# Kernel tuning notes

Hardware: AMD Instinct MI355X
Metric: run time of the kernel (lower is better)

Reference implementation:

```python
import jax, jax.numpy as jnp
import numpy as np

V = 50000   # vocab_size == output_size
E = 256     # emb_size
H = 512     # hidden_size
B = 128     # batch_size
L = 400     # encoder seq len
T = 100     # decoder history len


def setup_inputs() -> dict:
    key = jax.random.key(0)
    ks = jax.random.split(key, 20)
    s = 0.02
    return {
        "inputs": jax.random.randint(ks[0], (1, B), 0, V),
        "hidden": jax.random.normal(ks[1], (1, B, H), jnp.float32),
        "encoder_hidden": jax.random.normal(ks[2], (L, B, H), jnp.float32),
        "encoder_lengths": jax.random.randint(ks[3], (B,), 0, L),
        "previous_weights": jax.random.normal(ks[4], (B, 1, L), jnp.float32),
        "decoder_hidden": jax.random.normal(ks[5], (T, B, H), jnp.float32),
        "encoder_inputs": jax.random.randint(ks[6], (L, B), 0, V),
        "time_step": 0,
        "emb": jax.random.normal(ks[7], (V, E), jnp.float32) * s,
        "W_ih": jax.random.normal(ks[8], (3 * H, E), jnp.float32) * s,
        "W_hh": jax.random.normal(ks[9], (3 * H, H), jnp.float32) * s,
        "b_ih": jnp.zeros((3 * H,), jnp.float32),
        "b_hh": jnp.zeros((3 * H,), jnp.float32),
        "W_ae": jax.random.normal(ks[10], (H, H), jnp.float32) * s,
        "b_ae": jnp.zeros((H,), jnp.float32),
        "W_ad": jax.random.normal(ks[11], (H, H), jnp.float32) * s,
        "b_ad": jnp.zeros((H,), jnp.float32),
        "W_ptr": jax.random.normal(ks[12], (1, 3 * H), jnp.float32) * s,
        "b_ptr": jnp.zeros((1,), jnp.float32),
        "W_out": jax.random.normal(ks[13], (V, 3 * H), jnp.float32) * s,
        "b_out": jnp.zeros((V,), jnp.float32),
    }


def _gru_step(x, h, W_ih, W_hh, b_ih, b_hh):
    # Single-step torch-style GRU. x: (B,E), h: (B,H)
    hsz = h.shape[-1]
    gi = x @ W_ih.T + b_ih          # (B, 3H)
    gh = h @ W_hh.T + b_hh          # (B, 3H)
    i_r, i_z, i_n = gi[:, :hsz], gi[:, hsz:2 * hsz], gi[:, 2 * hsz:]
    h_r, h_z, h_n = gh[:, :hsz], gh[:, hsz:2 * hsz], gh[:, 2 * hsz:]
    r = jax.nn.sigmoid(i_r + h_r)
    z = jax.nn.sigmoid(i_z + h_z)
    n = jnp.tanh(i_n + r * h_n)
    return (1.0 - z) * n + z * h


def reference(inputs, hidden, encoder_hidden, encoder_lengths, previous_weights,
              decoder_hidden, encoder_inputs, time_step,
              emb, W_ih, W_hh, b_ih, b_hh, W_ae, b_ae, W_ad, b_ad,
              W_ptr, b_ptr, W_out, b_out):
    x = emb[inputs[0]]                       # (B,E)
    h = _gru_step(x, hidden[0], W_ih, W_hh, b_ih, b_hh)   # (B,H) == h_t_d

    enc_len = encoder_hidden.shape[0]
    # encoder attention
    te = h @ W_ae.T + b_ae                   # (B,H)
    e_t = jnp.einsum('bh,lbh->bl', te, encoder_hidden)    # (B,L)
    # faithful reproduction of source mask loop (empty slice -> effectively no-op)
    cond = (enc_len < encoder_lengths)[:, None] & (jnp.arange(enc_len)[None, :] >= encoder_lengths[:, None])
    e_t = jnp.where(cond, -jnp.inf, e_t)
    alpha_e = jax.nn.softmax(e_t, axis=-1)                # (B,L)
    c_t_e = jnp.einsum('bl,lbh->bh', alpha_e, encoder_hidden)

    # decoder (intra) attention
    td = h @ W_ad.T + b_ad
    e_t_d = jnp.einsum('bh,tbh->bt', td, decoder_hidden)  # (B,T)
    alpha_d = jax.nn.softmax(e_t_d, axis=-1)
    c_t_d = jnp.einsum('bt,tbh->bh', alpha_d, decoder_hidden)

    new_hidden = jnp.concatenate([c_t_e, h, c_t_d], axis=-1)   # (B,3H)
    gen = jax.nn.log_softmax(new_hidden @ W_out.T + b_out, axis=-1)  # (B,V)
    pointer_prob = new_hidden @ W_ptr.T + b_ptr                      # (B,1)

    enc_in = encoder_inputs.T                                        # (B,L) int
    alpha_scaled = pointer_prob * alpha_e                            # (B,L)
    vsz = W_out.shape[0]
    bidx = jnp.arange(enc_in.shape[0])[:, None]
    pointer_mask = jnp.zeros((enc_in.shape[0], vsz), gen.dtype).at[bidx, enc_in].add(alpha_scaled)

    final_output = (1.0 - pointer_prob) * gen + pointer_mask         # (B,V)
    return final_output, h[None], previous_weights
```

## Files before the change

### kernel.cpp

```cpp
#include <hip/hip_runtime.h>
#include <cstdint>
#include <cstddef>

#define VV 50000
#define EE 256
#define HH 512
#define BB 128
#define LL 400
#define TT 100
#define H3 1536

typedef __attribute__((ext_vector_type(8))) short short8;
typedef __attribute__((ext_vector_type(4))) float floatx4;

__device__ __forceinline__ unsigned short f2bf(float x) {
    union { float f; unsigned u; } v; v.f = x;
    unsigned r = v.u + 0x7fffu + ((v.u >> 16) & 1u);
    return (unsigned short)(r >> 16);
}

struct GemmJob {
    const float* A;
    const float* W;
    const float* bias;
    float*       C;
    int          lda;
    int          K;
};

#define GBN 64
#define GBK 32

__global__ __launch_bounds__(256) void gemm_m128(GemmJob j0, GemmJob j1,
                                                 int N, int ldc)
{
    GemmJob j = (blockIdx.y == 0) ? j0 : j1;
    __shared__ float As[GBK][128];
    __shared__ float Wls[GBK][GBN];

    const int tid = threadIdx.x;
    const int n0  = blockIdx.x * GBN;
    const int tx  = tid & 15;
    const int ty  = tid >> 4;
    const int kq  = tid & 7;
    const int arow = (tid >> 3) * 4;
    const int wrow = (tid >> 3) * 2;

    float acc[8][4];
    #pragma unroll
    for (int i = 0; i < 8; i++)
        #pragma unroll
        for (int jj = 0; jj < 4; jj++) acc[i][jj] = 0.f;

    for (int k0 = 0; k0 < j.K; k0 += GBK) {
        #pragma unroll
        for (int i = 0; i < 4; i++) {
            const float4 v = *(const float4*)(j.A + (size_t)(arow + i) * j.lda + k0 + kq * 4);
            As[kq*4+0][arow+i] = v.x;
            As[kq*4+1][arow+i] = v.y;
            As[kq*4+2][arow+i] = v.z;
            As[kq*4+3][arow+i] = v.w;
        }
        #pragma unroll
        for (int i = 0; i < 2; i++) {
            const int n = n0 + wrow + i;
            float4 v = make_float4(0.f, 0.f, 0.f, 0.f);
            if (n < N) v = *(const float4*)(j.W + (size_t)n * j.K + k0 + kq * 4);
            Wls[kq*4+0][wrow+i] = v.x;
            Wls[kq*4+1][wrow+i] = v.y;
            Wls[kq*4+2][wrow+i] = v.z;
            Wls[kq*4+3][wrow+i] = v.w;
        }
        __syncthreads();
        #pragma unroll
        for (int kk = 0; kk < GBK; kk++) {
            float a[8], w[4];
            #pragma unroll
            for (int i = 0; i < 8; i++) a[i] = As[kk][ty*8+i];
            #pragma unroll
            for (int jj = 0; jj < 4; jj++) w[jj] = Wls[kk][tx*4+jj];
            #pragma unroll
            for (int i = 0; i < 8; i++)
                #pragma unroll
                for (int jj = 0; jj < 4; jj++)
                    acc[i][jj] += a[i] * w[jj];
        }
        __syncthreads();
    }

    const int nbase = n0 + tx * 4;
    #pragma unroll
    for (int i = 0; i < 8; i++) {
        const int b = ty * 8 + i;
        if (nbase + 3 < N) {
            const float4 bb = *(const float4*)(j.bias + nbase);
            float4 r;
            r.x = acc[i][0] + bb.x;
            r.y = acc[i][1] + bb.y;
            r.z = acc[i][2] + bb.z;
            r.w = acc[i][3] + bb.w;
            *(float4*)(j.C + (size_t)b * ldc + nbase) = r;
        } else {
            #pragma unroll
            for (int jj = 0; jj < 4; jj++) {
                const int n = nbase + jj;
                if (n < N) j.C[(size_t)b * ldc + n] = acc[i][jj] + j.bias[n];
            }
        }
    }
}

__global__ __launch_bounds__(256) void vocab_mfma(const unsigned short* __restrict__ A,
                                                  const float* __restrict__ W,
                                                  const float* __restrict__ bias,
                                                  float* __restrict__ C)
{
    const int wave = threadIdx.x >> 6;
    const int lane = threadIdx.x & 63;
    const int quad = lane >> 4;
    const int nl   = lane & 15;
    const int n    = blockIdx.x * 64 + wave * 16 + nl;
    const int nc   = (n < VV) ? n : (VV - 1);

    floatx4 acc[8];
    #pragma unroll
    for (int i = 0; i < 8; i++) acc[i] = (floatx4){0.f, 0.f, 0.f, 0.f};

    const float* wp = W + (size_t)nc * H3 + quad * 8;
    const unsigned short* ap = A + (size_t)nl * H3 + quad * 8;

    for (int k0 = 0; k0 < H3; k0 += 32) {
        const float4 w0 = *(const float4*)(wp + k0);
        const float4 w1 = *(const float4*)(wp + k0 + 4);
        short8 bfrag;
        bfrag[0] = (short)f2bf(w0.x);
        bfrag[1] = (short)f2bf(w0.y);
        bfrag[2] = (short)f2bf(w0.z);
        bfrag[3] = (short)f2bf(w0.w);
        bfrag[4] = (short)f2bf(w1.x);
        bfrag[5] = (short)f2bf(w1.y);
        bfrag[6] = (short)f2bf(w1.z);
        bfrag[7] = (short)f2bf(w1.w);
        #pragma unroll
        for (int mt = 0; mt < 8; mt++) {
            const short8 af = *(const short8*)(ap + (size_t)mt * 16 * H3 + k0);
            acc[mt] = __builtin_amdgcn_mfma_f32_16x16x32_bf16(af, bfrag, acc[mt], 0, 0, 0);
        }
    }

    if (n < VV) {
        const float bv = bias[n];
        #pragma unroll
        for (int mt = 0; mt < 8; mt++) {
            #pragma unroll
            for (int r = 0; r < 4; r++) {
                const int m = mt * 16 + quad * 4 + r;
                C[(size_t)m * VV + n] = acc[mt][r] + bv;
            }
        }
    }
}

__global__ __launch_bounds__(256) void nh_to_bf16(const float* __restrict__ nh,
                                                  unsigned short* __restrict__ out)
{
    const int idx = blockIdx.x * 256 + threadIdx.x;
    out[idx] = f2bf(nh[idx]);
}

__global__ __launch_bounds__(256) void gather_emb(const int* __restrict__ tok,
                                                  const float* __restrict__ emb,
                                                  float* __restrict__ x)
{
    const int b = blockIdx.x;
    x[(size_t)b * EE + threadIdx.x] = emb[(size_t)tok[b] * EE + threadIdx.x];
}

__global__ __launch_bounds__(256) void zero_ctx(float* __restrict__ nh)
{
    float* p = nh + (size_t)blockIdx.x * H3;
    const int tid = threadIdx.x;
    p[tid] = 0.f;  p[tid + 256] = 0.f;
    p[1024 + tid] = 0.f;  p[1280 + tid] = 0.f;
}

__global__ __launch_bounds__(256) void gru_combine(const float* __restrict__ gi,
                                                   const float* __restrict__ gh,
                                                   const float* __restrict__ hprev,
                                                   float* __restrict__ nh,
                                                   float* __restrict__ out_h)
{
    const int b = blockIdx.x;
    const int tid = threadIdx.x;
    #pragma unroll
    for (int r = 0; r < 2; r++) {
        const int i = tid + r * 256;
        const size_t base = (size_t)b * H3;
        const float ir = gi[base + i],        hr = gh[base + i];
        const float iz = gi[base + 512 + i],  hz = gh[base + 512 + i];
        const float in_ = gi[base + 1024 + i], hn = gh[base + 1024 + i];
        const float rr = 1.f / (1.f + expf(-(ir + hr)));
        const float zz = 1.f / (1.f + expf(-(iz + hz)));
        const float nn = tanhf(in_ + rr * hn);
        const float hp = hprev[(size_t)b * HH + i];
        const float h  = (1.f - zz) * nn + zz * hp;
        nh[base + 512 + i] = h;
        out_h[(size_t)b * HH + i] = h;
    }
}

__global__ __launch_bounds__(256) void attn_scores(const float* __restrict__ q,
                                                   const float* __restrict__ ctx,
                                                   const int* __restrict__ lens,
                                                   float* __restrict__ out,
                                                   int Lc)
{
    const int b = blockIdx.y;
    const int wave = threadIdx.x >> 6;
    const int lane = threadIdx.x & 63;
    const int l = blockIdx.x * 4 + wave;
    const float4* q4 = (const float4*)(q + (size_t)b * HH);
    const float4* c4 = (const float4*)(ctx + ((size_t)l * BB + b) * HH);
    const float4 a0 = q4[lane],      b0 = c4[lane];
    const float4 a1 = q4[lane + 64], b1 = c4[lane + 64];
    float s = a0.x*b0.x + a0.y*b0.y + a0.z*b0.z + a0.w*b0.w
            + a1.x*b1.x + a1.y*b1.y + a1.z*b1.z + a1.w*b1.w;
    #pragma unroll
    for (int off = 32; off; off >>= 1)
        s += __shfl_down(s, off);
    if (lane == 0) {
        if (lens && (Lc < lens[b]) && (l >= lens[b])) s = -__builtin_inff();
        out[(size_t)b * Lc + l] = s;
    }
}

__global__ __launch_bounds__(256) void softmax2(float* __restrict__ ae, int ne,
                                                float* __restrict__ ad, int nd)
{
    __shared__ float red[256];
    const int tid = threadIdx.x;
    float* row;
    int n;
    if (blockIdx.y == 0) { row = ae + (size_t)blockIdx.x * ne; n = ne; }
    else                 { row = ad + (size_t)blockIdx.x * nd; n = nd; }

    float m = -__builtin_inff();
    for (int i = tid; i < n; i += 256) m = fmaxf(m, row[i]);
    red[tid] = m; __syncthreads();
    for (int s = 128; s; s >>= 1) {
        if (tid < s) red[tid] = fmaxf(red[tid], red[tid + s]);
        __syncthreads();
    }
    m = red[0]; __syncthreads();

    float sum = 0.f;
    for (int i = tid; i < n; i += 256) sum += expf(row[i] - m);
    red[tid] = sum; __syncthreads();
    for (int s = 128; s; s >>= 1) {
        if (tid < s) red[tid] += red[tid + s];
        __syncthreads();
    }
    const float inv = 1.f / red[0];
    for (int i = tid; i < n; i += 256) row[i] = expf(row[i] - m) * inv;
}

__global__ __launch_bounds__(256) void attn_context(const float* __restrict__ alpha,
                                                    const float* __restrict__ ctx,
                                                    float* __restrict__ dst,
                                                    int Lc, int chunk, int off)
{
    __shared__ float al[32];
    const int b = blockIdx.y;
    const int l0 = blockIdx.x * chunk;
    const int tid = threadIdx.x;
    if (tid < chunk) al[tid] = alpha[(size_t)b * Lc + l0 + tid];
    __syncthreads();
    float ax = 0.f, ay = 0.f;
    for (int ll = 0; ll < chunk; ll++) {
        const float2* c = (const float2*)(ctx + ((size_t)(l0 + ll) * BB + b) * HH);
        const float2 v = c[tid];
        const float w = al[ll];
        ax += w * v.x;
        ay += w * v.y;
    }
    atomicAdd(&dst[(size_t)b * H3 + off + tid * 2 + 0], ax);
    atomicAdd(&dst[(size_t)b * H3 + off + tid * 2 + 1], ay);
}

__global__ __launch_bounds__(256) void pointer_kernel(const float* __restrict__ nh,
                                                      const float* __restrict__ W_ptr,
                                                      const float* __restrict__ b_ptr,
                                                      float* __restrict__ pp)
{
    __shared__ float red[256];
    const int b = blockIdx.x;
    const int tid = threadIdx.x;
    float s = 0.f;
    for (int jj = tid; jj < H3; jj += 256) s += nh[(size_t)b * H3 + jj] * W_ptr[jj];
    red[tid] = s; __syncthreads();
    for (int t = 128; t; t >>= 1) {
        if (tid < t) red[tid] += red[tid + t];
        __syncthreads();
    }
    if (tid == 0) pp[b] = red[0] + b_ptr[0];
}

#define LSE_CHUNKS 10
#define LSE_SPAN 5000

__global__ __launch_bounds__(256) void lse_part(const float* __restrict__ logits,
                                                float2* __restrict__ part)
{
    __shared__ float rm[256], rs[256];
    const int b = blockIdx.y;
    const int s = blockIdx.x;
    const int tid = threadIdx.x;
    const float4* row = (const float4*)(logits + (size_t)b * VV + (size_t)s * LSE_SPAN);
    float m = -__builtin_inff(), sum = 0.f;
    for (int i = tid; i < LSE_SPAN / 4; i += 256) {
        const float4 v = row[i];
        const float mx = fmaxf(fmaxf(v.x, v.y), fmaxf(v.z, v.w));
        if (mx > m) { sum *= expf(m - mx); m = mx; }
        sum += expf(v.x - m) + expf(v.y - m) + expf(v.z - m) + expf(v.w - m);
    }
    rm[tid] = m; rs[tid] = sum; __syncthreads();
    for (int t = 128; t; t >>= 1) {
        if (tid < t) {
            const float m2 = rm[tid + t], s2 = rs[tid + t];
            const float M = fmaxf(rm[tid], m2);
            rs[tid] = rs[tid] * expf(rm[tid] - M) + s2 * expf(m2 - M);
            rm[tid] = M;
        }
        __syncthreads();
    }
    if (tid == 0) part[(size_t)b * LSE_CHUNKS + s] = make_float2(rm[0], rs[0]);
}

__global__ __launch_bounds__(128) void lse_final(const float2* __restrict__ part,
                                                 float* __restrict__ lse)
{
    const int b = threadIdx.x;
    float m = -__builtin_inff(), s = 0.f;
    #pragma unroll
    for (int i = 0; i < LSE_CHUNKS; i++) {
        const float2 p = part[(size_t)b * LSE_CHUNKS + i];
        const float M = fmaxf(m, p.x);
        s = s * expf(m - M) + p.y * expf(p.x - M);
        m = M;
    }
    lse[b] = m + logf(s);
}

__global__ __launch_bounds__(256) void final_write(float* __restrict__ out,
                                                   const float* __restrict__ pp,
                                                   const float* __restrict__ lse)
{
    const int b = blockIdx.y;
    const int v = (blockIdx.x * 256 + threadIdx.x) * 4;
    if (v >= VV) return;
    float4* p = (float4*)(out + (size_t)b * VV + v);
    float4 x = *p;
    const float g = 1.f - pp[b];
    const float Lse = lse[b];
    x.x = g * (x.x - Lse);
    x.y = g * (x.y - Lse);
    x.z = g * (x.z - Lse);
    x.w = g * (x.w - Lse);
    *p = x;
}

__global__ __launch_bounds__(256) void scatter_pointer(float* __restrict__ out,
                                                       const float* __restrict__ pp,
                                                       const float* __restrict__ alpha_e,
                                                       const int* __restrict__ enc_in)
{
    const int idx = blockIdx.x * 256 + threadIdx.x;
    if (idx >= BB * LL) return;
    const int b = idx / LL;
    const int l = idx - b * LL;
    const int tok = enc_in[(size_t)l * BB + b];
    atomicAdd(&out[(size_t)b * VV + tok], pp[b] * alpha_e[idx]);
}

__global__ __launch_bounds__(256) void copy_pw(float* __restrict__ dst,
                                               const float* __restrict__ src)
{
    const int idx = blockIdx.x * 256 + threadIdx.x;
    if (idx < BB * LL) dst[idx] = src[idx];
}

extern "C" void kernel_launch(void* const* d_in, const int* in_sizes, int n_in,
                              void* d_out, int out_size, void* d_ws, size_t ws_size,
                              hipStream_t stream)
{
    const int*   inputs  = (const int*)  d_in[0];
    const float* hidden  = (const float*)d_in[1];
    const float* enc_h   = (const float*)d_in[2];
    const int*   enc_len = (const int*)  d_in[3];
    const float* prev_w  = (const float*)d_in[4];
    const float* dec_h   = (const float*)d_in[5];
    const int*   enc_in  = (const int*)  d_in[6];
    const float* emb     = (const float*)d_in[8];
    const float* W_ih    = (const float*)d_in[9];
    const float* W_hh    = (const float*)d_in[10];
    const float* b_ih    = (const float*)d_in[11];
    const float* b_hh    = (const float*)d_in[12];
    const float* W_ae    = (const float*)d_in[13];
    const float* b_ae    = (const float*)d_in[14];
    const float* W_ad    = (const float*)d_in[15];
    const float* b_ad    = (const float*)d_in[16];
    const float* W_ptr   = (const float*)d_in[17];
    const float* b_ptr   = (const float*)d_in[18];
    const float* W_out   = (const float*)d_in[19];
    const float* b_out   = (const float*)d_in[20];

    float* out = (float*)d_out;
    float* out_final = out;
    float* out_h     = out + (size_t)BB * VV;
    float* out_pw    = out_h + (size_t)BB * HH;

    float* ws  = (float*)d_ws;
    float* X   = ws;
    float* GI  = X   + BB * EE;
    float* GH  = GI  + BB * H3;
    float* TE  = GH  + BB * H3;
    float* TD  = TE  + BB * HH;
    float* AE  = TD  + BB * HH;
    float* AD  = AE  + BB * LL;
    float* NH  = AD  + BB * TT;
    float* PP  = NH  + BB * H3;
    float* LSE = PP  + BB;
    float2* PART = (float2*)(LSE + BB);
    unsigned short* ABF = (unsigned short*)(PART + BB * LSE_CHUNKS);

    gather_emb<<<BB, 256, 0, stream>>>(inputs, emb, X);
    zero_ctx<<<BB, 256, 0, stream>>>(NH);

    {
        GemmJob jgi{X,      W_ih, b_ih, GI, EE, EE};
        GemmJob jgh{hidden, W_hh, b_hh, GH, HH, HH};
        gemm_m128<<<dim3(H3 / GBN, 2), 256, 0, stream>>>(jgi, jgh, H3, H3);
    }
    gru_combine<<<BB, 256, 0, stream>>>(GI, GH, hidden, NH, out_h);

    {
        GemmJob jte{NH + 512, W_ae, b_ae, TE, H3, HH};
        GemmJob jtd{NH + 512, W_ad, b_ad, TD, H3, HH};
        gemm_m128<<<dim3(HH / GBN, 2), 256, 0, stream>>>(jte, jtd, HH, HH);
    }

    attn_scores<<<dim3(LL / 4, BB), 256, 0, stream>>>(TE, enc_h, enc_len, AE, LL);
    attn_scores<<<dim3(TT / 4, BB), 256, 0, stream>>>(TD, dec_h, nullptr, AD, TT);

    softmax2<<<dim3(BB, 2), 256, 0, stream>>>(AE, LL, AD, TT);

    attn_context<<<dim3(LL / 25, BB), 256, 0, stream>>>(AE, enc_h, NH, LL, 25, 0);
    attn_context<<<dim3(TT / 25, BB), 256, 0, stream>>>(AD, dec_h, NH, TT, 25, 1024);

    pointer_kernel<<<BB, 256, 0, stream>>>(NH, W_ptr, b_ptr, PP);

    nh_to_bf16<<<(BB * H3) / 256, 256, 0, stream>>>(NH, ABF);
    vocab_mfma<<<(VV + 63) / 64, 256, 0, stream>>>(ABF, W_out, b_out, out_final);

    lse_part<<<dim3(LSE_CHUNKS, BB), 256, 0, stream>>>(out_final, PART);
    lse_final<<<1, 128, 0, stream>>>(PART, LSE);
    final_write<<<dim3((VV / 4 + 255) / 256, BB), 256, 0, stream>>>(out_final, PP, LSE);

    scatter_pointer<<<(BB * LL) / 256, 256, 0, stream>>>(out_final, PP, AE, enc_in);

    copy_pw<<<(BB * LL) / 256, 256, 0, stream>>>(out_pw, prev_w);
}
```

Measured before the change: 907.6 us.

## Fuse small kernels and software-pipeline loads in vocab MFMA GEMM

Merges several small launches: gather and zeroing into one prep kernel, encoder and decoder attention score and context kernels into single launches, the bf16 conversion into the pointer kernel, lse_final into final_write, and the prev-weights copy into the scatter. The vocab projection GEMM now prefetches the next K-slice of weights and activations into registers before issuing the current MFMAs, and packs fp32 to bf16 with a byte-permute. The bf16 packing changes from round-to-nearest-even to round-half-up, which slightly alters rounding. Every row block in final_write now recomputes the log-sum-exp combine redundantly.

```diff
diff --git a/kernel.cpp b/kernel.cpp
--- a/kernel.cpp
+++ b/kernel.cpp
@@ -17,6 +17,14 @@
     union { float f; unsigned u; } v; v.f = x;
     unsigned r = v.u + 0x7fffu + ((v.u >> 16) & 1u);
     return (unsigned short)(r >> 16);
+}
+
+__device__ __forceinline__ unsigned bfpack(float x, float y) {
+    union { float f; unsigned u; } a, b;
+    a.f = x; b.f = y;
+    const unsigned lo = a.u + 0x8000u;
+    const unsigned hi = b.u + 0x8000u;
+    return __builtin_amdgcn_perm(hi, lo, 0x07060302u);
 }
 
 struct GemmJob {
@@ -129,23 +137,37 @@
     const float* wp = W + (size_t)nc * H3 + quad * 8;
     const unsigned short* ap = A + (size_t)nl * H3 + quad * 8;
 
+    float4 cw0 = *(const float4*)(wp);
+    float4 cw1 = *(const float4*)(wp + 4);
+    short8 caf[8];
+    #pragma unroll
+    for (int mt = 0; mt < 8; mt++)
+        caf[mt] = *(const short8*)(ap + (size_t)mt * 16 * H3);
+
     for (int k0 = 0; k0 < H3; k0 += 32) {
-        const float4 w0 = *(const float4*)(wp + k0);
-        const float4 w1 = *(const float4*)(wp + k0 + 4);
-        short8 bfrag;
-        bfrag[0] = (short)f2bf(w0.x);
-        bfrag[1] = (short)f2bf(w0.y);
-        bfrag[2] = (short)f2bf(w0.z);
-        bfrag[3] = (short)f2bf(w0.w);
-        bfrag[4] = (short)f2bf(w1.x);
-        bfrag[5] = (short)f2bf(w1.y);
-        bfrag[6] = (short)f2bf(w1.z);
-        bfrag[7] = (short)f2bf(w1.w);
-        #pragma unroll
-        for (int mt = 0; mt < 8; mt++) {
-            const short8 af = *(const short8*)(ap + (size_t)mt * 16 * H3 + k0);
-            acc[mt] = __builtin_amdgcn_mfma_f32_16x16x32_bf16(af, bfrag, acc[mt], 0, 0, 0);
-        }
+        int k1 = k0 + 32;
+        k1 = (k1 < H3) ? k1 : 0;
+        const float4 nw0 = *(const float4*)(wp + k1);
+        const float4 nw1 = *(const float4*)(wp + k1 + 4);
+        short8 naf[8];
+        #pragma unroll
+        for (int mt = 0; mt < 8; mt++)
+            naf[mt] = *(const short8*)(ap + (size_t)mt * 16 * H3 + k1);
+
+        int4 bi;
+        bi.x = (int)bfpack(cw0.x, cw0.y);
+        bi.y = (int)bfpack(cw0.z, cw0.w);
+        bi.z = (int)bfpack(cw1.x, cw1.y);
+        bi.w = (int)bfpack(cw1.z, cw1.w);
+        const short8 bf = *(const short8*)&bi;
+
+        #pragma unroll
+        for (int mt = 0; mt < 8; mt++)
+            acc[mt] = __builtin_amdgcn_mfma_f32_16x16x32_bf16(caf[mt], bf, acc[mt], 0, 0, 0);
+
+        cw0 = nw0; cw1 = nw1;
+        #pragma unroll
+        for (int mt = 0; mt < 8; mt++) caf[mt] = naf[mt];
     }
 
     if (n < VV) {
@@ -161,25 +183,15 @@
     }
 }
 
-__global__ __launch_bounds__(256) void nh_to_bf16(const float* __restrict__ nh,
-                                                  unsigned short* __restrict__ out)
-{
-    const int idx = blockIdx.x * 256 + threadIdx.x;
-    out[idx] = f2bf(nh[idx]);
-}
-
-__global__ __launch_bounds__(256) void gather_emb(const int* __restrict__ tok,
-                                                  const float* __restrict__ emb,
-                                                  float* __restrict__ x)
+__global__ __launch_bounds__(256) void prep(const int* __restrict__ tok,
+                                            const float* __restrict__ emb,
+                                            float* __restrict__ x,
+                                            float* __restrict__ nh)
 {
     const int b = blockIdx.x;
-    x[(size_t)b * EE + threadIdx.x] = emb[(size_t)tok[b] * EE + threadIdx.x];
-}
-
-__global__ __launch_bounds__(256) void zero_ctx(float* __restrict__ nh)
-{
-    float* p = nh + (size_t)blockIdx.x * H3;
-    const int tid = threadIdx.x;
+    const int tid = threadIdx.x;
+    x[(size_t)b * EE + tid] = emb[(size_t)tok[b] * EE + tid];
+    float* p = nh + (size_t)b * H3;
     p[tid] = 0.f;  p[tid + 256] = 0.f;
     p[1024 + tid] = 0.f;  p[1280 + tid] = 0.f;
 }
@@ -209,18 +221,33 @@
     }
 }
 
-__global__ __launch_bounds__(256) void attn_scores(const float* __restrict__ q,
-                                                   const float* __restrict__ ctx,
-                                                   const int* __restrict__ lens,
-                                                   float* __restrict__ out,
-                                                   int Lc)
+__global__ __launch_bounds__(256) void attn_scores2(const float* __restrict__ qe,
+                                                    const float* __restrict__ ctxe,
+                                                    const int* __restrict__ lens,
+                                                    float* __restrict__ oute,
+                                                    const float* __restrict__ qd,
+                                                    const float* __restrict__ ctxd,
+                                                    float* __restrict__ outd)
 {
     const int b = blockIdx.y;
     const int wave = threadIdx.x >> 6;
     const int lane = threadIdx.x & 63;
-    const int l = blockIdx.x * 4 + wave;
+
+    const float* q;
+    const float* c;
+    float* o;
+    int l, Lc;
+    bool mask;
+    if (blockIdx.x < 100) {
+        l = blockIdx.x * 4 + wave; Lc = LL;
+        q = qe; c = ctxe; o = oute; mask = true;
+    } else {
+        l = (blockIdx.x - 100) * 4 + wave; Lc = TT;
+        q = qd; c = ctxd; o = outd; mask = false;
+    }
+
     const float4* q4 = (const float4*)(q + (size_t)b * HH);
-    const float4* c4 = (const float4*)(ctx + ((size_t)l * BB + b) * HH);
+    const float4* c4 = (const float4*)(c + ((size_t)l * BB + b) * HH);
     const float4 a0 = q4[lane],      b0 = c4[lane];
     const float4 a1 = q4[lane + 64], b1 = c4[lane + 64];
     float s = a0.x*b0.x + a0.y*b0.y + a0.z*b0.z + a0.w*b0.w
@@ -229,8 +256,8 @@
     for (int off = 32; off; off >>= 1)
         s += __shfl_down(s, off);
     if (lane == 0) {
-        if (lens && (Lc < lens[b]) && (l >= lens[b])) s = -__builtin_inff();
-        out[(size_t)b * Lc + l] = s;
+        if (mask && (Lc < lens[b]) && (l >= lens[b])) s = -__builtin_inff();
+        o[(size_t)b * Lc + l] = s;
     }
 }
 
@@ -264,19 +291,32 @@
     for (int i = tid; i < n; i += 256) row[i] = expf(row[i] - m) * inv;
 }
 
-__global__ __launch_bounds__(256) void attn_context(const float* __restrict__ alpha,
-                                                    const float* __restrict__ ctx,
-                                                    float* __restrict__ dst,
-                                                    int Lc, int chunk, int off)
+__global__ __launch_bounds__(256) void attn_context2(const float* __restrict__ ae,
+                                                     const float* __restrict__ ctxe,
+                                                     const float* __restrict__ ad,
+                                                     const float* __restrict__ ctxd,
+                                                     float* __restrict__ dst)
 {
     __shared__ float al[32];
     const int b = blockIdx.y;
-    const int l0 = blockIdx.x * chunk;
-    const int tid = threadIdx.x;
-    if (tid < chunk) al[tid] = alpha[(size_t)b * Lc + l0 + tid];
+    const int tid = threadIdx.x;
+
+    const float* alpha;
+    const float* ctx;
+    int l0, Lc, off;
+    if (blockIdx.x < 16) {
+        l0 = blockIdx.x * 25; Lc = LL; off = 0;
+        alpha = ae; ctx = ctxe;
+    } else {
+        l0 = (blockIdx.x - 16) * 25; Lc = TT; off = 1024;
+        alpha = ad; ctx = ctxd;
+    }
+
+    if (tid < 25) al[tid] = alpha[(size_t)b * Lc + l0 + tid];
     __syncthreads();
     float ax = 0.f, ay = 0.f;
-    for (int ll = 0; ll < chunk; ll++) {
+    #pragma unroll 5
+    for (int ll = 0; ll < 25; ll++) {
         const float2* c = (const float2*)(ctx + ((size_t)(l0 + ll) * BB + b) * HH);
         const float2 v = c[tid];
         const float w = al[ll];
@@ -287,16 +327,23 @@
     atomicAdd(&dst[(size_t)b * H3 + off + tid * 2 + 1], ay);
 }
 
-__global__ __launch_bounds__(256) void pointer_kernel(const float* __restrict__ nh,
-                                                      const float* __restrict__ W_ptr,
-                                                      const float* __restrict__ b_ptr,
-                                                      float* __restrict__ pp)
+__global__ __launch_bounds__(256) void pointer_bf16(const float* __restrict__ nh,
+                                                    const float* __restrict__ W_ptr,
+                                                    const float* __restrict__ b_ptr,
+                                                    float* __restrict__ pp,
+                                                    unsigned short* __restrict__ abf)
 {
     __shared__ float red[256];
     const int b = blockIdx.x;
     const int tid = threadIdx.x;
     float s = 0.f;
-    for (int jj = tid; jj < H3; jj += 256) s += nh[(size_t)b * H3 + jj] * W_ptr[jj];
+    #pragma unroll
+    for (int r = 0; r < 6; r++) {
+        const int jj = tid + r * 256;
+        const float v = nh[(size_t)b * H3 + jj];
+        abf[(size_t)b * H3 + jj] = f2bf(v);
+        s += v * W_ptr[jj];
+    }
     red[tid] = s; __syncthreads();
     for (int t = 128; t; t >>= 1) {
         if (tid < t) red[tid] += red[tid + t];
@@ -336,10 +383,11 @@
     if (tid == 0) part[(size_t)b * LSE_CHUNKS + s] = make_float2(rm[0], rs[0]);
 }
 
-__global__ __launch_bounds__(128) void lse_final(const float2* __restrict__ part,
-                                                 float* __restrict__ lse)
-{
-    const int b = threadIdx.x;
+__global__ __launch_bounds__(256) void final_write(float* __restrict__ out,
+                                                   const float* __restrict__ pp,
+                                                   const float2* __restrict__ part)
+{
+    const int b = blockIdx.y;
     float m = -__builtin_inff(), s = 0.f;
     #pragma unroll
     for (int i = 0; i < LSE_CHUNKS; i++) {
@@ -348,20 +396,13 @@
         s = s * expf(m - M) + p.y * expf(p.x - M);
         m = M;
     }
-    lse[b] = m + logf(s);
-}
-
-__global__ __launch_bounds__(256) void final_write(float* __restrict__ out,
-                                                   const float* __restrict__ pp,
-                                                   const float* __restrict__ lse)
-{
-    const int b = blockIdx.y;
+    const float Lse = m + logf(s);
+
     const int v = (blockIdx.x * 256 + threadIdx.x) * 4;
     if (v >= VV) return;
     float4* p = (float4*)(out + (size_t)b * VV + v);
     float4 x = *p;
     const float g = 1.f - pp[b];
-    const float Lse = lse[b];
     x.x = g * (x.x - Lse);
     x.y = g * (x.y - Lse);
     x.z = g * (x.z - Lse);
@@ -369,24 +410,20 @@
     *p = x;
 }
 
-__global__ __launch_bounds__(256) void scatter_pointer(float* __restrict__ out,
-                                                       const float* __restrict__ pp,
-                                                       const float* __restrict__ alpha_e,
-                                                       const int* __restrict__ enc_in)
+__global__ __launch_bounds__(256) void scatter_copy(float* __restrict__ out,
+                                                    const float* __restrict__ pp,
+                                                    const float* __restrict__ alpha_e,
+                                                    const int* __restrict__ enc_in,
+                                                    float* __restrict__ pw_dst,
+                                                    const float* __restrict__ pw_src)
 {
     const int idx = blockIdx.x * 256 + threadIdx.x;
     if (idx >= BB * LL) return;
+    pw_dst[idx] = pw_src[idx];
     const int b = idx / LL;
     const int l = idx - b * LL;
     const int tok = enc_in[(size_t)l * BB + b];
     atomicAdd(&out[(size_t)b * VV + tok], pp[b] * alpha_e[idx]);
-}
-
-__global__ __launch_bounds__(256) void copy_pw(float* __restrict__ dst,
-                                               const float* __restrict__ src)
-{
-    const int idx = blockIdx.x * 256 + threadIdx.x;
-    if (idx < BB * LL) dst[idx] = src[idx];
 }
 
 extern "C" void kernel_launch(void* const* d_in, const int* in_sizes, int n_in,
@@ -433,8 +470,7 @@
     float2* PART = (float2*)(LSE + BB);
     unsigned short* ABF = (unsigned short*)(PART + BB * LSE_CHUNKS);
 
-    gather_emb<<<BB, 256, 0, stream>>>(inputs, emb, X);
-    zero_ctx<<<BB, 256, 0, stream>>>(NH);
+    prep<<<BB, 256, 0, stream>>>(inputs, emb, X, NH);
 
     {
         GemmJob jgi{X,      W_ih, b_ih, GI, EE, EE};
@@ -449,24 +485,20 @@
         gemm_m128<<<dim3(HH / GBN, 2), 256, 0, stream>>>(jte, jtd, HH, HH);
     }
 
-    attn_scores<<<dim3(LL / 4, BB), 256, 0, stream>>>(TE, enc_h, enc_len, AE, LL);
-    attn_scores<<<dim3(TT / 4, BB), 256, 0, stream>>>(TD, dec_h, nullptr, AD, TT);
+    attn_scores2<<<dim3(125, BB), 256, 0, stream>>>(TE, enc_h, enc_len, AE,
+                                                    TD, dec_h, AD);
 
     softmax2<<<dim3(BB, 2), 256, 0, stream>>>(AE, LL, AD, TT);
 
-    attn_context<<<dim3(LL / 25, BB), 256, 0, stream>>>(AE, enc_h, NH, LL, 25, 0);
-    attn_context<<<dim3(TT / 25, BB), 256, 0, stream>>>(AD, dec_h, NH, TT, 25, 1024);
-
-    pointer_kernel<<<BB, 256, 0, stream>>>(NH, W_ptr, b_ptr, PP);
-
-    nh_to_bf16<<<(BB * H3) / 256, 256, 0, stream>>>(NH, ABF);
+    attn_context2<<<dim3(20, BB), 256, 0, stream>>>(AE, enc_h, AD, dec_h, NH);
+
+    pointer_bf16<<<BB, 256, 0, stream>>>(NH, W_ptr, b_ptr, PP, ABF);
+
     vocab_mfma<<<(VV + 63) / 64, 256, 0, stream>>>(ABF, W_out, b_out, out_final);
 
     lse_part<<<dim3(LSE_CHUNKS, BB), 256, 0, stream>>>(out_final, PART);
-    lse_final<<<1, 128, 0, stream>>>(PART, LSE);
-    final_write<<<dim3((VV / 4 + 255) / 256, BB), 256, 0, stream>>>(out_final, PP, LSE);
-
-    scatter_pointer<<<(BB * LL) / 256, 256, 0, stream>>>(out_final, PP, AE, enc_in);
-
-    copy_pw<<<(BB * LL) / 256, 256, 0, stream>>>(out_pw, prev_w);
-}
+    final_write<<<dim3((VV / 4 + 255) / 256, BB), 256, 0, stream>>>(out_final, PP, PART);
+
+    scatter_copy<<<(BB * LL) / 256, 256, 0, stream>>>(out_final, PP, AE, enc_in,
+                                                      out_pw, prev_w);
+}
```

Measured after the change: 875.2 us. 1.04x faster.
